# Performance work log

Hardware: AMD Instinct MI355X
Metric: run time of the kernel (lower is better)

Reference implementation:

```python
import jax, jax.numpy as jnp
import numpy as np

B, S, E, H = 4, 2048, 1024, 16
D = E // H  # head_dim = 64
ROPE_BASE = 10000.0


def _rope(x):
    # x: [B, H, S, D] -> rotary position embedding applied over seq dim
    seq_len = x.shape[2]
    inv_freq = 1.0 / (ROPE_BASE ** (jnp.arange(0, D, 2, dtype=jnp.float32) / D))  # [D/2]
    freqs = jnp.arange(seq_len, dtype=jnp.float32)[:, None] * inv_freq[None, :]   # [S, D/2]
    emb = jnp.concatenate([freqs, freqs], axis=-1)                                 # [S, D]
    cos = jnp.cos(emb).astype(x.dtype)
    sin = jnp.sin(emb).astype(x.dtype)
    x1, x2 = jnp.split(x, 2, axis=-1)
    rotated = jnp.concatenate([-x2, x1], axis=-1)
    return x * cos + rotated * sin


def setup_inputs() -> dict:
    key = jax.random.key(0)
    ks = jax.random.split(key, 10)
    p = 0.02
    return {
        "x": jax.random.normal(ks[0], (B, S, E), dtype=jnp.float32),
        "Wq": jax.random.normal(ks[1], (E, E), dtype=jnp.float32) * p,
        "bq": jnp.zeros((E,), dtype=jnp.float32),
        "Wk": jax.random.normal(ks[2], (E, E), dtype=jnp.float32) * p,
        "bk": jnp.zeros((E,), dtype=jnp.float32),
        "Wv": jax.random.normal(ks[3], (E, E), dtype=jnp.float32) * p,
        "bv": jnp.zeros((E,), dtype=jnp.float32),
        "Wo": jax.random.normal(ks[4], (E, E), dtype=jnp.float32) * p,
        "bo": jnp.zeros((E,), dtype=jnp.float32),
        "key_padding_mask": jnp.zeros((B, S), dtype=bool),
    }


def reference(x, Wq, bq, Wk, bk, Wv, bv, Wo, bo, key_padding_mask):
    b, s, _ = x.shape
    # QKV projections -> [B, H, S, D]
    def proj(W, bias):
        return (x @ W + bias).reshape(b, s, H, D).transpose(0, 2, 1, 3)
    q = _rope(proj(Wq, bq))
    k = _rope(proj(Wk, bk))
    v = proj(Wv, bv)
    scale = D ** -0.5
    scores = jnp.einsum('bhqd,bhkd->bhqk', q, k) * scale  # [B, H, S, S]
    scores = jnp.where(key_padding_mask[:, None, None, :], jnp.finfo(scores.dtype).min, scores)
    probs = jax.nn.softmax(scores, axis=-1)
    out = jnp.einsum('bhqk,bhkd->bhqd', probs, v)         # [B, H, S, D]
    out = out.transpose(0, 2, 1, 3).reshape(b, s, E)
    return out @ Wo + bo
```

## Files before the change

### kernel.cpp

```cpp
#include <hip/hip_runtime.h>
#include <hip/hip_bf16.h>
#include <math.h>

#define Bn 4
#define Sn 2048
#define En 1024
#define Hn 16
#define Dn 64
#define Mn (Bn * Sn)

typedef __attribute__((ext_vector_type(8))) short short8;
typedef __attribute__((ext_vector_type(4))) short short4v;
typedef __attribute__((ext_vector_type(4))) float f32x4;
typedef __attribute__((ext_vector_type(16))) float f32x16;
typedef __attribute__((ext_vector_type(2))) unsigned int uint2v;

#if __has_builtin(__builtin_amdgcn_exp2f)
#define EXP2(x) __builtin_amdgcn_exp2f(x)
#else
#define EXP2(x) exp2f(x)
#endif

#if __has_builtin(__builtin_amdgcn_permlane32_swap)
#define HAVE_PLSWAP 1
#endif

#define GLOAD16(g, s) __builtin_amdgcn_global_load_lds( \
    (const __attribute__((address_space(1))) unsigned int*)(g), \
    (__attribute__((address_space(3))) unsigned int*)(s), 16, 0, 0)

__device__ inline unsigned short f2bf(float f) {
    unsigned int u = __float_as_uint(f);
    u += 0x7FFFu + ((u >> 16) & 1u);
    return (unsigned short)(u >> 16);
}
__device__ inline float bf2f(unsigned short h) {
    return __uint_as_float(((unsigned int)h) << 16);
}
__device__ inline void split2(float f, unsigned short& hi, unsigned short& lo) {
    hi = f2bf(f);
    lo = f2bf(f - bf2f(hi));
}
__device__ inline short8 ld8s(const unsigned short* p) {
    union { short4v h[2]; short8 v; } r;
    r.h[0] = *(const short4v*)p;
    r.h[1] = *(const short4v*)(p + 4);
    return r.v;
}
__device__ inline short8 g8(const unsigned short* p) {
    union { int4 i; short8 v; } r;
    r.i = *(const int4*)p;
    return r.v;
}

__device__ inline void st16(unsigned short* base, int row, int col16, int4 v) {
    const unsigned off = ((unsigned)(row * 128 + col16 * 2)) ^ ((unsigned)((row & 7) << 4));
    *(int4*)((char*)base + off) = v;
}
__device__ inline short8 ld16(const unsigned short* base, int row, int col16) {
    const unsigned off = ((unsigned)(row * 128 + col16 * 2)) ^ ((unsigned)((row & 7) << 4));
    union { int4 i; short8 v; } r;
    r.i = *(const int4*)((const char*)base + off);
    return r.v;
}

__global__ __launch_bounds__(256) void convx_kernel(
    const float* __restrict__ X, unsigned short* __restrict__ Xh) {
    int i = blockIdx.x * 256 + threadIdx.x;
    float4 v = ((const float4*)X)[i];
    float f[4] = {v.x, v.y, v.z, v.w};
    short4v h;
#pragma unroll
    for (int j = 0; j < 4; ++j) h[j] = (short)f2bf(f[j]);
    ((short4v*)Xh)[i] = h;
}

__global__ __launch_bounds__(256) void tconv5_kernel(
    const float* __restrict__ Wq, const float* __restrict__ Wk,
    const float* __restrict__ Wv, const float* __restrict__ Wo,
    unsigned short* __restrict__ WqkvT, unsigned short* __restrict__ WoT2,
    float* __restrict__ ct, float* __restrict__ st) {
    const int m = blockIdx.z;
    if (m == 4) {
        const int i = (blockIdx.y * 16 + blockIdx.x) * 256 + threadIdx.x;
        const int s = i >> 5, p = i & 31;
        double inv = pow(10000.0, -(double)p / 32.0);
        double a = (double)s * inv;
        ct[i] = (float)cos(a);
        st[i] = (float)sin(a);
        return;
    }
    const float* W = (m == 0) ? Wq : (m == 1) ? Wk : (m == 2) ? Wv : Wo;
    unsigned short* dst = (m < 3) ? WqkvT + (size_t)m * En * En : WoT2;
    const int rowLen = (m < 3) ? En : 2048;
    const int dup = (m == 3);

    __shared__ float Ws[64][65];
    const int t = threadIdx.x;
    const int kb = blockIdx.y * 64, nb = blockIdx.x * 64;
    const int lr = t >> 2, lc = (t & 3) * 16;
#pragma unroll
    for (int u = 0; u < 4; ++u) {
        float4 v = *(const float4*)&W[(size_t)(kb + lr) * En + nb + lc + 4 * u];
        Ws[lr][lc + 4 * u + 0] = v.x; Ws[lr][lc + 4 * u + 1] = v.y;
        Ws[lr][lc + 4 * u + 2] = v.z; Ws[lr][lc + 4 * u + 3] = v.w;
    }
    __syncthreads();
    const int orow = t >> 2, ock = (t & 3) * 16;
#pragma unroll
    for (int u = 0; u < 4; ++u) {
        short4v hs;
#pragma unroll
        for (int j = 0; j < 4; ++j) hs[j] = (short)f2bf(Ws[ock + 4 * u + j][orow]);
        unsigned short* dp = &dst[(size_t)(nb + orow) * rowLen + kb + ock + 4 * u];
        *(short4v*)dp = hs;
        if (dup) *(short4v*)(dp + 1024) = hs;
    }
}

__global__ __launch_bounds__(256) void vtrans_kernel(
    const unsigned short* __restrict__ Vb, unsigned short* __restrict__ VbT) {
    __shared__ unsigned short Ts[64][68];
    const int t = threadIdx.x;
    const int bh = blockIdx.y;
    const int s0 = blockIdx.x * 64;
    const size_t ibase = (size_t)bh * Sn * Dn;
    const int lr = t >> 2, lc = (t & 3) * 16;
    int4 i0 = *(const int4*)&Vb[ibase + (size_t)(s0 + lr) * Dn + lc];
    int4 i1 = *(const int4*)&Vb[ibase + (size_t)(s0 + lr) * Dn + lc + 8];
    *(int2*)&Ts[lr][lc] = make_int2(i0.x, i0.y);
    *(int2*)&Ts[lr][lc + 4] = make_int2(i0.z, i0.w);
    *(int2*)&Ts[lr][lc + 8] = make_int2(i1.x, i1.y);
    *(int2*)&Ts[lr][lc + 12] = make_int2(i1.z, i1.w);
    __syncthreads();
    const int dr = t >> 2, sc = (t & 3) * 16;
    unsigned short o[16];
#pragma unroll
    for (int j = 0; j < 16; ++j) o[j] = Ts[sc + j][dr];
    unsigned short* op = &VbT[(size_t)bh * Dn * Sn + (size_t)dr * Sn + s0 + sc];
    *(int4*)&op[0] = *(int4*)&o[0];
    *(int4*)&op[8] = *(int4*)&o[8];
}

template <int KN, int EPI>
__global__ __launch_bounds__(256) void gemm97(
    const unsigned short* __restrict__ A, const unsigned short* __restrict__ Bt,
    const float* __restrict__ b0, const float* __restrict__ bkv,
    const float* __restrict__ bvv,
    unsigned short* __restrict__ oQ, unsigned short* __restrict__ oK,
    unsigned short* __restrict__ oV, float* __restrict__ oF,
    const float* __restrict__ ct, const float* __restrict__ st) {
    __shared__ unsigned short As[128][64];
    __shared__ unsigned short Bs[128][64];
    const int t = threadIdx.x;
    const int w = t >> 6, l = t & 63;
    const int wm = w & 1, wn = w >> 1;
    const int q = l >> 4, ln16 = l & 15;
    const int r8 = l >> 3, i8 = l & 7;

    int bx = blockIdx.x, by = blockIdx.y;
    {
        const int gx = gridDim.x;
        const int nwg = gx * gridDim.y;
        if ((nwg & 7) == 0) {
            const int n = by * gx + bx;
            const int s = (n & 7) * (nwg >> 3) + (n >> 3);
            bx = s % gx; by = s / gx;
        }
    }
    const int m0 = by * 128, n0 = bx * 128;

    f32x4 acc[4][4];
#pragma unroll
    for (int i = 0; i < 4; ++i)
#pragma unroll
        for (int j = 0; j < 4; ++j)
#pragma unroll
            for (int r = 0; r < 4; ++r) acc[i][j][r] = 0.0f;

    const unsigned short* Ag = &A[(size_t)(m0 + 32 * w + r8) * KN + 8 * i8];
    const unsigned short* Bg = &Bt[(size_t)(n0 + 32 * w + r8) * KN + 8 * i8];

    for (int k0 = 0; k0 < KN; k0 += 64) {
        __syncthreads();
#pragma unroll
        for (int j = 0; j < 4; ++j) {
            GLOAD16(Ag + (size_t)(8 * j) * KN + k0, &As[32 * w + 8 * j][0]);
            GLOAD16(Bg + (size_t)(8 * j) * KN + k0, &Bs[32 * w + 8 * j][0]);
        }
        __syncthreads();
#pragma unroll
        for (int ks = 0; ks < 2; ++ks) {
            short8 af[4], bf[4];
#pragma unroll
            for (int i = 0; i < 4; ++i)
                af[i] = ld8s(&As[64 * wm + 16 * i + ln16][32 * ks + 8 * q]);
#pragma unroll
            for (int j = 0; j < 4; ++j)
                bf[j] = ld8s(&Bs[64 * wn + 16 * j + ln16][32 * ks + 8 * q]);
#pragma unroll
            for (int i = 0; i < 4; ++i)
#pragma unroll
                for (int j = 0; j < 4; ++j)
                    acc[i][j] = __builtin_amdgcn_mfma_f32_16x16x32_bf16(
                        af[i], bf[j], acc[i][j], 0, 0, 0);
        }
    }

    if (EPI == 0) {
#pragma unroll
        for (int i = 0; i < 4; ++i)
#pragma unroll
            for (int r = 0; r < 4; ++r) {
                const int m = m0 + 64 * wm + 16 * i + 4 * q + r;
#pragma unroll
                for (int j = 0; j < 4; ++j) {
                    const int n = n0 + 64 * wn + 16 * j + ln16;
                    oF[(size_t)m * En + n] = acc[i][j][r] + b0[n];
                }
            }
    } else {
        const int mat = n0 >> 10;
        const int nIn = (n0 & 1023) + 64 * wn;
        const int hh = nIn >> 6;
        const float* bias = (mat == 0) ? b0 : (mat == 1) ? bkv : bvv;
        unsigned short* op = (mat == 0) ? oQ : (mat == 1) ? oK : oV;
#pragma unroll
        for (int i = 0; i < 4; ++i)
#pragma unroll
            for (int r = 0; r < 4; ++r) {
                const int m = m0 + 64 * wm + 16 * i + 4 * q + r;
                const int b = m >> 11, s2 = m & (Sn - 1);
                const size_t base = (((size_t)(b * Hn + hh)) * Sn + s2) * Dn;
#pragma unroll
                for (int j = 0; j < 2; ++j) {
                    const int nh = 16 * j + ln16;
                    float v0 = acc[i][j][r] + bias[nIn + nh];
                    float v1 = acc[i][j + 2][r] + bias[nIn + nh + 32];
                    if (mat <= 1) {
                        float c = ct[s2 * 32 + nh], sn = st[s2 * 32 + nh];
                        float o0 = v0 * c - v1 * sn;
                        float o1 = v1 * c + v0 * sn;
                        if (mat == 0) {
                            o0 *= 0.18033688011112042f;
                            o1 *= 0.18033688011112042f;
                        }
                        v0 = o0; v1 = o1;
                    }
                    op[base + nh] = f2bf(v0);
                    op[base + nh + 32] = f2bf(v1);
                }
            }
    }
}

__global__ __launch_bounds__(256) void attn_mfma_kernel(
    const unsigned short* __restrict__ Qb, const unsigned short* __restrict__ Kb,
    const unsigned short* __restrict__ VbT, const unsigned char* __restrict__ mask,
    unsigned short* __restrict__ Obuf) {
    __shared__ __align__(16) unsigned short Ks[2][64][64];
    __shared__ __align__(16) unsigned short Vs[2][64][64];

    const int t = threadIdx.x;
    const int w = t >> 6, l = t & 63, h2 = l >> 5, ln = l & 31;
    const int q0 = blockIdx.x * 128;
    const int h = blockIdx.y, b = blockIdx.z;
    const size_t ho = ((size_t)(b * Hn + h)) * Sn * Dn;
    const unsigned char* maskB = mask + (size_t)b * Sn;

    short8 qh[4];
    const int qrow = q0 + 32 * w + ln;
#pragma unroll
    for (int s = 0; s < 4; ++s)
        qh[s] = g8(&Qb[ho + (size_t)qrow * Dn + 16 * s + 8 * h2]);

    f32x16 accO0, accO1;
#pragma unroll
    for (int i = 0; i < 16; ++i) { accO0[i] = 0.0f; accO1[i] = 0.0f; }
    float lsum[4] = {0.0f, 0.0f, 0.0f, 0.0f};

    const int kr = t >> 2, kc = (t & 3) * 16;
    const unsigned short* Kp = &Kb[ho + (size_t)kr * Dn + kc];
    const unsigned short* Vp = &VbT[ho + (size_t)kr * Sn + kc];

    int4 ck0 = *(const int4*)Kp, ck1 = *(const int4*)(Kp + 8);
    int4 cv0 = *(const int4*)Vp, cv1 = *(const int4*)(Vp + 8);
    unsigned char cm = maskB[l];

#pragma unroll 2
    for (int kt = 0; kt < Sn / 64; ++kt) {
        const int pb = kt & 1;
        unsigned short* KsP = &Ks[pb][0][0];
        unsigned short* VsP = &Vs[pb][0][0];
        st16(KsP, kr, kc, ck0); st16(KsP, kr, kc + 8, ck1);
        st16(VsP, kr, kc, cv0); st16(VsP, kr, kc + 8, cv1);
        const unsigned long long bm = __ballot(cm != 0);
        __syncthreads();
        const int kn = ((kt + 1) & (Sn / 64 - 1)) * 64;
        ck0 = *(const int4*)(Kp + (size_t)kn * Dn);
        ck1 = *(const int4*)(Kp + (size_t)kn * Dn + 8);
        cv0 = *(const int4*)(Vp + kn);
        cv1 = *(const int4*)(Vp + kn + 8);
        cm = maskB[kn + l];

#pragma unroll
        for (int c = 0; c < 2; ++c) {
            short8 kf[4];
#pragma unroll
            for (int s = 0; s < 4; ++s)
                kf[s] = ld16(KsP, 32 * c + ln, 16 * s + 8 * h2);
            f32x16 accS;
#pragma unroll
            for (int i = 0; i < 16; ++i) accS[i] = 0.0f;
            __builtin_amdgcn_s_setprio(1);
#pragma unroll
            for (int s = 0; s < 4; ++s)
                accS = __builtin_amdgcn_mfma_f32_32x32x16_bf16(kf[s], qh[s], accS, 0, 0, 0);
            __builtin_amdgcn_s_setprio(0);

            unsigned pw[8];
#pragma unroll
            for (int g = 0; g < 4; ++g)
#pragma unroll
                for (int j = 0; j < 2; ++j) {
                    const int r0 = 4 * g + 2 * j;
                    float p0 = EXP2(accS[r0]);
                    float p1 = EXP2(accS[r0 + 1]);
                    if (bm) {
                        const int key = 32 * c + 8 * g + 4 * h2 + 2 * j;
                        if ((bm >> key) & 1) p0 = 0.0f;
                        if ((bm >> (key + 1)) & 1) p1 = 0.0f;
                    }
                    lsum[g] += p0 + p1;
                    union { __hip_bfloat162 h; unsigned u; } cv;
                    cv.h = __float22bfloat162_rn(make_float2(p0, p1));
                    pw[2 * g + j] = cv.u;
                }

#pragma unroll
            for (int s = 0; s < 2; ++s) {
                union { unsigned u[4]; short8 v; } af;
#ifdef HAVE_PLSWAP
                uint2v r02 = __builtin_amdgcn_permlane32_swap(
                    pw[4 * s + 0], pw[4 * s + 2], false, false);
                uint2v r13 = __builtin_amdgcn_permlane32_swap(
                    pw[4 * s + 1], pw[4 * s + 3], false, false);
                af.u[0] = r02[0]; af.u[1] = r13[0];
                af.u[2] = r02[1]; af.u[3] = r13[1];
#else
                const unsigned x0 = pw[4 * s + 0], x1 = pw[4 * s + 1];
                const unsigned y0 = pw[4 * s + 2], y1 = pw[4 * s + 3];
                const unsigned py0 = (unsigned)__shfl_xor((int)y0, 32);
                const unsigned py1 = (unsigned)__shfl_xor((int)y1, 32);
                const unsigned px0 = (unsigned)__shfl_xor((int)x0, 32);
                const unsigned px1 = (unsigned)__shfl_xor((int)x1, 32);
                af.u[0] = h2 ? py0 : x0;
                af.u[1] = h2 ? py1 : x1;
                af.u[2] = h2 ? y0 : px0;
                af.u[3] = h2 ? y1 : px1;
#endif
                short8 vA = ld16(VsP, ln, 32 * c + 16 * s + 8 * h2);
                short8 vB = ld16(VsP, 32 + ln, 32 * c + 16 * s + 8 * h2);
                __builtin_amdgcn_s_setprio(1);
                accO0 = __builtin_amdgcn_mfma_f32_32x32x16_bf16(af.v, vA, accO0, 0, 0, 0);
                accO1 = __builtin_amdgcn_mfma_f32_32x32x16_bf16(af.v, vB, accO1, 0, 0, 0);
                __builtin_amdgcn_s_setprio(0);
            }
        }
    }

    const float lme = (lsum[0] + lsum[1]) + (lsum[2] + lsum[3]);
    const float tot = lme + __shfl_xor(lme, 32);
    const float linv = 1.0f / fmaxf(tot, 1e-37f);
#pragma unroll
    for (int r = 0; r < 16; ++r) {
        const int row = (r & 3) + 8 * (r >> 2) + 4 * h2;
        const float lr = __shfl(linv, row);
        const int s = q0 + 32 * w + row;
        const size_t base = ((size_t)b * Sn + s) * 2048 + h * Dn;
        unsigned short a, b2;
        split2(accO0[r] * lr, a, b2);
        Obuf[base + ln] = a; Obuf[base + 1024 + ln] = b2;
        split2(accO1[r] * lr, a, b2);
        Obuf[base + 32 + ln] = a; Obuf[base + 1024 + 32 + ln] = b2;
    }
}

extern "C" void kernel_launch(void* const* d_in, const int* in_sizes, int n_in,
                              void* d_out, int out_size, void* d_ws, size_t ws_size,
                              hipStream_t stream) {
    const float* x  = (const float*)d_in[0];
    const float* Wq = (const float*)d_in[1];
    const float* bq = (const float*)d_in[2];
    const float* Wk = (const float*)d_in[3];
    const float* bk = (const float*)d_in[4];
    const float* Wv = (const float*)d_in[5];
    const float* bv = (const float*)d_in[6];
    const float* Wo = (const float*)d_in[7];
    const float* bo = (const float*)d_in[8];
    const unsigned char* mask = (const unsigned char*)d_in[9];

    const size_t NE = (size_t)Mn * En;
    const size_t WN = (size_t)En * En;
    unsigned short* ws = (unsigned short*)d_ws;
    unsigned short* Xh = ws;
    unsigned short* Qb = Xh + NE;
    unsigned short* Kb = Qb + NE;
    unsigned short* Vb = Kb + NE;
    unsigned short* VbT = Vb + NE;
    unsigned short* Obuf = VbT + NE;
    unsigned short* WqkvT = Obuf + 2 * NE;
    unsigned short* WoT2 = WqkvT + 3 * WN;
    float* ct = (float*)(WoT2 + 2 * WN);
    float* st = ct + (size_t)Sn * 32;

    convx_kernel<<<(int)(NE / 1024), 256, 0, stream>>>(x, Xh);
    tconv5_kernel<<<dim3(16, 16, 5), 256, 0, stream>>>(
        Wq, Wk, Wv, Wo, WqkvT, WoT2, ct, st);

    gemm97<En, 1><<<dim3(3 * En / 128, Mn / 128), 256, 0, stream>>>(
        Xh, WqkvT, bq, bk, bv, Qb, Kb, Vb, nullptr, ct, st);

    vtrans_kernel<<<dim3(Sn / 64, Bn * Hn), 256, 0, stream>>>(Vb, VbT);

    attn_mfma_kernel<<<dim3(Sn / 128, Hn, Bn), 256, 0, stream>>>(
        Qb, Kb, VbT, mask, Obuf);

    gemm97<2048, 0><<<dim3(En / 128, Mn / 128), 256, 0, stream>>>(
        Obuf, WoT2, bo, nullptr, nullptr, nullptr, nullptr, nullptr,
        (float*)d_out, ct, st);
}
```

Before: 346.1 us.

## Process two query tiles per wave in attention to reuse K/V fragments

Each wave now handles 64 query rows (two 32-row MFMA tiles) instead of 32, doubling the block's query tile to 256 and halving the grid. K and V fragments loaded from LDS are reused across both tiles, which halves LDS traffic and global K/V loads per query. Probability packing to bf16 now truncates instead of rounding, and the row sum accumulates the truncated values so it matches what the PV MFMA sees. The cost is more accumulator registers per thread and fewer blocks (512), which may lower occupancy and leave CUs less evenly loaded.

Result: slower. 382.0 us (+10.4%).

```diff
diff --git a/kernel.cpp b/kernel.cpp
--- a/kernel.cpp
+++ b/kernel.cpp
@@ -254,6 +254,52 @@
     }
 }
 
+__device__ inline void softpack(const f32x16& accS, unsigned long long bm,
+                                int c, int h2, float* lsum, unsigned* pw) {
+#pragma unroll
+    for (int g = 0; g < 4; ++g)
+#pragma unroll
+        for (int j = 0; j < 2; ++j) {
+            const int r0 = 4 * g + 2 * j;
+            float p0 = EXP2(accS[r0]);
+            float p1 = EXP2(accS[r0 + 1]);
+            if (bm) {
+                const int key = 32 * c + 8 * g + 4 * h2 + 2 * j;
+                if ((bm >> key) & 1) p0 = 0.0f;
+                if ((bm >> (key + 1)) & 1) p1 = 0.0f;
+            }
+            const unsigned u0 = __float_as_uint(p0) & 0xFFFF0000u;
+            const unsigned u1 = __float_as_uint(p1) & 0xFFFF0000u;
+            lsum[g] += __uint_as_float(u0);
+            lsum[g] += __uint_as_float(u1);
+            pw[2 * g + j] = (u0 >> 16) | u1;
+        }
+}
+
+__device__ inline short8 pv_afrag(const unsigned* pw, int s, int h2) {
+    union { unsigned u[4]; short8 v; } af;
+#ifdef HAVE_PLSWAP
+    uint2v r02 = __builtin_amdgcn_permlane32_swap(
+        pw[4 * s + 0], pw[4 * s + 2], false, false);
+    uint2v r13 = __builtin_amdgcn_permlane32_swap(
+        pw[4 * s + 1], pw[4 * s + 3], false, false);
+    af.u[0] = r02[0]; af.u[1] = r13[0];
+    af.u[2] = r02[1]; af.u[3] = r13[1];
+#else
+    const unsigned x0 = pw[4 * s + 0], x1 = pw[4 * s + 1];
+    const unsigned y0 = pw[4 * s + 2], y1 = pw[4 * s + 3];
+    const unsigned py0 = (unsigned)__shfl_xor((int)y0, 32);
+    const unsigned py1 = (unsigned)__shfl_xor((int)y1, 32);
+    const unsigned px0 = (unsigned)__shfl_xor((int)x0, 32);
+    const unsigned px1 = (unsigned)__shfl_xor((int)x1, 32);
+    af.u[0] = h2 ? py0 : x0;
+    af.u[1] = h2 ? py1 : x1;
+    af.u[2] = h2 ? y0 : px0;
+    af.u[3] = h2 ? y1 : px1;
+#endif
+    return af.v;
+}
+
 __global__ __launch_bounds__(256) void attn_mfma_kernel(
     const unsigned short* __restrict__ Qb, const unsigned short* __restrict__ Kb,
     const unsigned short* __restrict__ VbT, const unsigned char* __restrict__ mask,
@@ -263,21 +309,24 @@
 
     const int t = threadIdx.x;
     const int w = t >> 6, l = t & 63, h2 = l >> 5, ln = l & 31;
-    const int q0 = blockIdx.x * 128;
+    const int q0 = blockIdx.x * 256;
     const int h = blockIdx.y, b = blockIdx.z;
     const size_t ho = ((size_t)(b * Hn + h)) * Sn * Dn;
     const unsigned char* maskB = mask + (size_t)b * Sn;
 
-    short8 qh[4];
-    const int qrow = q0 + 32 * w + ln;
-#pragma unroll
-    for (int s = 0; s < 4; ++s)
-        qh[s] = g8(&Qb[ho + (size_t)qrow * Dn + 16 * s + 8 * h2]);
-
-    f32x16 accO0, accO1;
-#pragma unroll
-    for (int i = 0; i < 16; ++i) { accO0[i] = 0.0f; accO1[i] = 0.0f; }
-    float lsum[4] = {0.0f, 0.0f, 0.0f, 0.0f};
+    short8 qhA[4], qhB[4];
+    const int qrA = q0 + 64 * w + ln;
+#pragma unroll
+    for (int s = 0; s < 4; ++s) {
+        qhA[s] = g8(&Qb[ho + (size_t)qrA * Dn + 16 * s + 8 * h2]);
+        qhB[s] = g8(&Qb[ho + (size_t)(qrA + 32) * Dn + 16 * s + 8 * h2]);
+    }
+
+    f32x16 aO0, aO1, bO0, bO1;
+#pragma unroll
+    for (int i = 0; i < 16; ++i) { aO0[i] = 0.0f; aO1[i] = 0.0f; bO0[i] = 0.0f; bO1[i] = 0.0f; }
+    float lsA[4] = {0.0f, 0.0f, 0.0f, 0.0f};
+    float lsB[4] = {0.0f, 0.0f, 0.0f, 0.0f};
 
     const int kr = t >> 2, kc = (t & 3) * 16;
     const unsigned short* Kp = &Kb[ho + (size_t)kr * Dn + kc];
@@ -309,80 +358,58 @@
 #pragma unroll
             for (int s = 0; s < 4; ++s)
                 kf[s] = ld16(KsP, 32 * c + ln, 16 * s + 8 * h2);
-            f32x16 accS;
-#pragma unroll
-            for (int i = 0; i < 16; ++i) accS[i] = 0.0f;
+            f32x16 aS, bS;
+#pragma unroll
+            for (int i = 0; i < 16; ++i) { aS[i] = 0.0f; bS[i] = 0.0f; }
             __builtin_amdgcn_s_setprio(1);
 #pragma unroll
-            for (int s = 0; s < 4; ++s)
-                accS = __builtin_amdgcn_mfma_f32_32x32x16_bf16(kf[s], qh[s], accS, 0, 0, 0);
+            for (int s = 0; s < 4; ++s) {
+                aS = __builtin_amdgcn_mfma_f32_32x32x16_bf16(kf[s], qhA[s], aS, 0, 0, 0);
+                bS = __builtin_amdgcn_mfma_f32_32x32x16_bf16(kf[s], qhB[s], bS, 0, 0, 0);
+            }
             __builtin_amdgcn_s_setprio(0);
 
-            unsigned pw[8];
-#pragma unroll
-            for (int g = 0; g < 4; ++g)
-#pragma unroll
-                for (int j = 0; j < 2; ++j) {
-                    const int r0 = 4 * g + 2 * j;
-                    float p0 = EXP2(accS[r0]);
-                    float p1 = EXP2(accS[r0 + 1]);
-                    if (bm) {
-                        const int key = 32 * c + 8 * g + 4 * h2 + 2 * j;
-                        if ((bm >> key) & 1) p0 = 0.0f;
-                        if ((bm >> (key + 1)) & 1) p1 = 0.0f;
-                    }
-                    lsum[g] += p0 + p1;
-                    union { __hip_bfloat162 h; unsigned u; } cv;
-                    cv.h = __float22bfloat162_rn(make_float2(p0, p1));
-                    pw[2 * g + j] = cv.u;
-                }
+            unsigned pwa[8], pwb[8];
+            softpack(aS, bm, c, h2, lsA, pwa);
+            softpack(bS, bm, c, h2, lsB, pwb);
 
 #pragma unroll
             for (int s = 0; s < 2; ++s) {
-                union { unsigned u[4]; short8 v; } af;
-#ifdef HAVE_PLSWAP
-                uint2v r02 = __builtin_amdgcn_permlane32_swap(
-                    pw[4 * s + 0], pw[4 * s + 2], false, false);
-                uint2v r13 = __builtin_amdgcn_permlane32_swap(
-                    pw[4 * s + 1], pw[4 * s + 3], false, false);
-                af.u[0] = r02[0]; af.u[1] = r13[0];
-                af.u[2] = r02[1]; af.u[3] = r13[1];
-#else
-                const unsigned x0 = pw[4 * s + 0], x1 = pw[4 * s + 1];
-                const unsigned y0 = pw[4 * s + 2], y1 = pw[4 * s + 3];
-                const unsigned py0 = (unsigned)__shfl_xor((int)y0, 32);
-                const unsigned py1 = (unsigned)__shfl_xor((int)y1, 32);
-                const unsigned px0 = (unsigned)__shfl_xor((int)x0, 32);
-                const unsigned px1 = (unsigned)__shfl_xor((int)x1, 32);
-                af.u[0] = h2 ? py0 : x0;
-                af.u[1] = h2 ? py1 : x1;
-                af.u[2] = h2 ? y0 : px0;
-                af.u[3] = h2 ? y1 : px1;
-#endif
+                short8 afA = pv_afrag(pwa, s, h2);
+                short8 afB = pv_afrag(pwb, s, h2);
                 short8 vA = ld16(VsP, ln, 32 * c + 16 * s + 8 * h2);
                 short8 vB = ld16(VsP, 32 + ln, 32 * c + 16 * s + 8 * h2);
                 __builtin_amdgcn_s_setprio(1);
-                accO0 = __builtin_amdgcn_mfma_f32_32x32x16_bf16(af.v, vA, accO0, 0, 0, 0);
-                accO1 = __builtin_amdgcn_mfma_f32_32x32x16_bf16(af.v, vB, accO1, 0, 0, 0);
+                aO0 = __builtin_amdgcn_mfma_f32_32x32x16_bf16(afA, vA, aO0, 0, 0, 0);
+                aO1 = __builtin_amdgcn_mfma_f32_32x32x16_bf16(afA, vB, aO1, 0, 0, 0);
+                bO0 = __builtin_amdgcn_mfma_f32_32x32x16_bf16(afB, vA, bO0, 0, 0, 0);
+                bO1 = __builtin_amdgcn_mfma_f32_32x32x16_bf16(afB, vB, bO1, 0, 0, 0);
                 __builtin_amdgcn_s_setprio(0);
             }
         }
     }
 
-    const float lme = (lsum[0] + lsum[1]) + (lsum[2] + lsum[3]);
-    const float tot = lme + __shfl_xor(lme, 32);
-    const float linv = 1.0f / fmaxf(tot, 1e-37f);
+    const float lmA = (lsA[0] + lsA[1]) + (lsA[2] + lsA[3]);
+    const float lmB = (lsB[0] + lsB[1]) + (lsB[2] + lsB[3]);
+    const float invA = 1.0f / fmaxf(lmA + __shfl_xor(lmA, 32), 1e-37f);
+    const float invB = 1.0f / fmaxf(lmB + __shfl_xor(lmB, 32), 1e-37f);
 #pragma unroll
     for (int r = 0; r < 16; ++r) {
         const int row = (r & 3) + 8 * (r >> 2) + 4 * h2;
-        const float lr = __shfl(linv, row);
-        const int s = q0 + 32 * w + row;
-        const size_t base = ((size_t)b * Sn + s) * 2048 + h * Dn;
-        unsigned short a, b2;
-        split2(accO0[r] * lr, a, b2);
-        Obuf[base + ln] = a; Obuf[base + 1024 + ln] = b2;
-        split2(accO1[r] * lr, a, b2);
-        Obuf[base + 32 + ln] = a; Obuf[base + 1024 + 32 + ln] = b2;
+        const float lrA = __shfl(invA, row);
+        const float lrB = __shfl(invB, row);
+        const int sA = q0 + 64 * w + row;
+        const size_t baseA = ((size_t)b * Sn + sA) * 2048 + h * Dn;
+        const size_t baseB = baseA + (size_t)32 * 2048;
+        unsigned short x, y;
+        split2(aO0[r] * lrA, x, y);
+        Obuf[baseA + ln] = x; Obuf[baseA + 1024 + ln] = y;
+        split2(aO1[r] * lrA, x, y);
+        Obuf[baseA + 32 + ln] = x; Obuf[baseA + 1024 + 32 + ln] = y;
+        split2(bO0[r] * lrB, x, y);
+        Obuf[baseB + ln] = x; Obuf[baseB + 1024 + ln] = y;
+        split2(bO1[r] * lrB, x, y);
+        Obuf[baseB + 32 + ln] = x; Obuf[baseB + 1024 + 32 + ln] = y;
     }
 }
 
@@ -423,7 +450,7 @@
 
     vtrans_kernel<<<dim3(Sn / 64, Bn * Hn), 256, 0, stream>>>(Vb, VbT);
 
-    attn_mfma_kernel<<<dim3(Sn / 128, Hn, Bn), 256, 0, stream>>>(
+    attn_mfma_kernel<<<dim3(Sn / 256, Hn, Bn), 256, 0, stream>>>(
         Qb, Kb, VbT, mask, Obuf);
 
     gemm97<2048, 0><<<dim3(En / 128, Mn / 128), 256, 0, stream>>>(
```

## Drop split-bf16 output projection and truncate softmax probabilities to bf16

Applied to the files above, without the earlier changes.

The attention output was previously stored as a hi/lo bf16 pair, with a duplicated Wo, so the output GEMM ran over K=2048 for extra precision. That GEMM now runs on a single bf16 copy with K=1024, which halves its MFMA work and the Obuf traffic. The softmax probabilities are also truncated to bf16 instead of rounded, and the row sum is built from the truncated values so it stays consistent with the packed operands. The main risk is lower accuracy in the final projection.

New measurement: 316.7 us. 1.09x faster.

```diff
diff --git a/kernel.cpp b/kernel.cpp
--- a/kernel.cpp
+++ b/kernel.cpp
@@ -37,10 +37,6 @@
 __device__ inline float bf2f(unsigned short h) {
     return __uint_as_float(((unsigned int)h) << 16);
 }
-__device__ inline void split2(float f, unsigned short& hi, unsigned short& lo) {
-    hi = f2bf(f);
-    lo = f2bf(f - bf2f(hi));
-}
 __device__ inline short8 ld8s(const unsigned short* p) {
     union { short4v h[2]; short8 v; } r;
     r.h[0] = *(const short4v*)p;
@@ -78,7 +74,7 @@
 __global__ __launch_bounds__(256) void tconv5_kernel(
     const float* __restrict__ Wq, const float* __restrict__ Wk,
     const float* __restrict__ Wv, const float* __restrict__ Wo,
-    unsigned short* __restrict__ WqkvT, unsigned short* __restrict__ WoT2,
+    unsigned short* __restrict__ WqkvT, unsigned short* __restrict__ WoT,
     float* __restrict__ ct, float* __restrict__ st) {
     const int m = blockIdx.z;
     if (m == 4) {
@@ -91,9 +87,7 @@
         return;
     }
     const float* W = (m == 0) ? Wq : (m == 1) ? Wk : (m == 2) ? Wv : Wo;
-    unsigned short* dst = (m < 3) ? WqkvT + (size_t)m * En * En : WoT2;
-    const int rowLen = (m < 3) ? En : 2048;
-    const int dup = (m == 3);
+    unsigned short* dst = (m < 3) ? WqkvT + (size_t)m * En * En : WoT;
 
     __shared__ float Ws[64][65];
     const int t = threadIdx.x;
@@ -112,9 +106,7 @@
         short4v hs;
 #pragma unroll
         for (int j = 0; j < 4; ++j) hs[j] = (short)f2bf(Ws[ock + 4 * u + j][orow]);
-        unsigned short* dp = &dst[(size_t)(nb + orow) * rowLen + kb + ock + 4 * u];
-        *(short4v*)dp = hs;
-        if (dup) *(short4v*)(dp + 1024) = hs;
+        *(short4v*)&dst[(size_t)(nb + orow) * En + kb + ock + 4 * u] = hs;
     }
 }
 
@@ -254,6 +246,52 @@
     }
 }
 
+__device__ inline void softpack(const f32x16& accS, unsigned long long bm,
+                                int c, int h2, float* lsum, unsigned* pw) {
+#pragma unroll
+    for (int g = 0; g < 4; ++g)
+#pragma unroll
+        for (int j = 0; j < 2; ++j) {
+            const int r0 = 4 * g + 2 * j;
+            float p0 = EXP2(accS[r0]);
+            float p1 = EXP2(accS[r0 + 1]);
+            if (bm) {
+                const int key = 32 * c + 8 * g + 4 * h2 + 2 * j;
+                if ((bm >> key) & 1) p0 = 0.0f;
+                if ((bm >> (key + 1)) & 1) p1 = 0.0f;
+            }
+            const unsigned u0 = __float_as_uint(p0) & 0xFFFF0000u;
+            const unsigned u1 = __float_as_uint(p1) & 0xFFFF0000u;
+            lsum[g] += __uint_as_float(u0);
+            lsum[g] += __uint_as_float(u1);
+            pw[2 * g + j] = (u0 >> 16) | u1;
+        }
+}
+
+__device__ inline short8 pv_afrag(const unsigned* pw, int s, int h2) {
+    union { unsigned u[4]; short8 v; } af;
+#ifdef HAVE_PLSWAP
+    uint2v r02 = __builtin_amdgcn_permlane32_swap(
+        pw[4 * s + 0], pw[4 * s + 2], false, false);
+    uint2v r13 = __builtin_amdgcn_permlane32_swap(
+        pw[4 * s + 1], pw[4 * s + 3], false, false);
+    af.u[0] = r02[0]; af.u[1] = r13[0];
+    af.u[2] = r02[1]; af.u[3] = r13[1];
+#else
+    const unsigned x0 = pw[4 * s + 0], x1 = pw[4 * s + 1];
+    const unsigned y0 = pw[4 * s + 2], y1 = pw[4 * s + 3];
+    const unsigned py0 = (unsigned)__shfl_xor((int)y0, 32);
+    const unsigned py1 = (unsigned)__shfl_xor((int)y1, 32);
+    const unsigned px0 = (unsigned)__shfl_xor((int)x0, 32);
+    const unsigned px1 = (unsigned)__shfl_xor((int)x1, 32);
+    af.u[0] = h2 ? py0 : x0;
+    af.u[1] = h2 ? py1 : x1;
+    af.u[2] = h2 ? y0 : px0;
+    af.u[3] = h2 ? y1 : px1;
+#endif
+    return af.v;
+}
+
 __global__ __launch_bounds__(256) void attn_mfma_kernel(
     const unsigned short* __restrict__ Qb, const unsigned short* __restrict__ Kb,
     const unsigned short* __restrict__ VbT, const unsigned char* __restrict__ mask,
@@ -319,51 +357,16 @@
             __builtin_amdgcn_s_setprio(0);
 
             unsigned pw[8];
-#pragma unroll
-            for (int g = 0; g < 4; ++g)
-#pragma unroll
-                for (int j = 0; j < 2; ++j) {
-                    const int r0 = 4 * g + 2 * j;
-                    float p0 = EXP2(accS[r0]);
-                    float p1 = EXP2(accS[r0 + 1]);
-                    if (bm) {
-                        const int key = 32 * c + 8 * g + 4 * h2 + 2 * j;
-                        if ((bm >> key) & 1) p0 = 0.0f;
-                        if ((bm >> (key + 1)) & 1) p1 = 0.0f;
-                    }
-                    lsum[g] += p0 + p1;
-                    union { __hip_bfloat162 h; unsigned u; } cv;
-                    cv.h = __float22bfloat162_rn(make_float2(p0, p1));
-                    pw[2 * g + j] = cv.u;
-                }
+            softpack(accS, bm, c, h2, lsum, pw);
 
 #pragma unroll
             for (int s = 0; s < 2; ++s) {
-                union { unsigned u[4]; short8 v; } af;
-#ifdef HAVE_PLSWAP
-                uint2v r02 = __builtin_amdgcn_permlane32_swap(
-                    pw[4 * s + 0], pw[4 * s + 2], false, false);
-                uint2v r13 = __builtin_amdgcn_permlane32_swap(
-                    pw[4 * s + 1], pw[4 * s + 3], false, false);
-                af.u[0] = r02[0]; af.u[1] = r13[0];
-                af.u[2] = r02[1]; af.u[3] = r13[1];
-#else
-                const unsigned x0 = pw[4 * s + 0], x1 = pw[4 * s + 1];
-                const unsigned y0 = pw[4 * s + 2], y1 = pw[4 * s + 3];
-                const unsigned py0 = (unsigned)__shfl_xor((int)y0, 32);
-                const unsigned py1 = (unsigned)__shfl_xor((int)y1, 32);
-                const unsigned px0 = (unsigned)__shfl_xor((int)x0, 32);
-                const unsigned px1 = (unsigned)__shfl_xor((int)x1, 32);
-                af.u[0] = h2 ? py0 : x0;
-                af.u[1] = h2 ? py1 : x1;
-                af.u[2] = h2 ? y0 : px0;
-                af.u[3] = h2 ? y1 : px1;
-#endif
+                short8 af = pv_afrag(pw, s, h2);
                 short8 vA = ld16(VsP, ln, 32 * c + 16 * s + 8 * h2);
                 short8 vB = ld16(VsP, 32 + ln, 32 * c + 16 * s + 8 * h2);
                 __builtin_amdgcn_s_setprio(1);
-                accO0 = __builtin_amdgcn_mfma_f32_32x32x16_bf16(af.v, vA, accO0, 0, 0, 0);
-                accO1 = __builtin_amdgcn_mfma_f32_32x32x16_bf16(af.v, vB, accO1, 0, 0, 0);
+                accO0 = __builtin_amdgcn_mfma_f32_32x32x16_bf16(af, vA, accO0, 0, 0, 0);
+                accO1 = __builtin_amdgcn_mfma_f32_32x32x16_bf16(af, vB, accO1, 0, 0, 0);
                 __builtin_amdgcn_s_setprio(0);
             }
         }
@@ -377,12 +380,9 @@
         const int row = (r & 3) + 8 * (r >> 2) + 4 * h2;
         const float lr = __shfl(linv, row);
         const int s = q0 + 32 * w + row;
-        const size_t base = ((size_t)b * Sn + s) * 2048 + h * Dn;
-        unsigned short a, b2;
-        split2(accO0[r] * lr, a, b2);
-        Obuf[base + ln] = a; Obuf[base + 1024 + ln] = b2;
-        split2(accO1[r] * lr, a, b2);
-        Obuf[base + 32 + ln] = a; Obuf[base + 1024 + 32 + ln] = b2;
+        const size_t base = ((size_t)b * Sn + s) * 1024 + h * Dn;
+        Obuf[base + ln] = f2bf(accO0[r] * lr);
+        Obuf[base + 32 + ln] = f2bf(accO1[r] * lr);
     }
 }
 
@@ -409,14 +409,14 @@
     unsigned short* Vb = Kb + NE;
     unsigned short* VbT = Vb + NE;
     unsigned short* Obuf = VbT + NE;
-    unsigned short* WqkvT = Obuf + 2 * NE;
-    unsigned short* WoT2 = WqkvT + 3 * WN;
-    float* ct = (float*)(WoT2 + 2 * WN);
+    unsigned short* WqkvT = Obuf + NE;
+    unsigned short* WoT = WqkvT + 3 * WN;
+    float* ct = (float*)(WoT + WN);
     float* st = ct + (size_t)Sn * 32;
 
     convx_kernel<<<(int)(NE / 1024), 256, 0, stream>>>(x, Xh);
     tconv5_kernel<<<dim3(16, 16, 5), 256, 0, stream>>>(
-        Wq, Wk, Wv, Wo, WqkvT, WoT2, ct, st);
+        Wq, Wk, Wv, Wo, WqkvT, WoT, ct, st);
 
     gemm97<En, 1><<<dim3(3 * En / 128, Mn / 128), 256, 0, stream>>>(
         Xh, WqkvT, bq, bk, bv, Qb, Kb, Vb, nullptr, ct, st);
@@ -426,7 +426,7 @@
     attn_mfma_kernel<<<dim3(Sn / 128, Hn, Bn), 256, 0, stream>>>(
         Qb, Kb, VbT, mask, Obuf);
 
-    gemm97<2048, 0><<<dim3(En / 128, Mn / 128), 256, 0, stream>>>(
-        Obuf, WoT2, bo, nullptr, nullptr, nullptr, nullptr, nullptr,
+    gemm97<En, 0><<<dim3(En / 128, Mn / 128), 256, 0, stream>>>(
+        Obuf, WoT, bo, nullptr, nullptr, nullptr, nullptr, nullptr,
         (float*)d_out, ct, st);
 }
```
